# Optimization experiments

Measured on AMD Instinct MI355X. Metric: run time of the kernel, lower is better.

## Reference

```python
import jax, jax.numpy as jnp
import numpy as np

B, T, H, F, E = 512, 32, 768, 3072, 3  # E = num_route_experts = num_experts - 1 (top-1 beam)


def setup_inputs() -> dict:
    key = jax.random.key(0)
    ks = jax.random.split(key, 4)
    s = 0.02
    return {
        "x": jax.random.normal(ks[0], (B, T, H), jnp.float32),
        "Wg": jax.random.normal(ks[1], (E, H), jnp.float32) * s,
        "W1": jax.random.normal(ks[2], (E, H, F), jnp.float32) * s,
        "b1": jnp.zeros((E, F), jnp.float32),
        "W2": jax.random.normal(ks[3], (E, F, H), jnp.float32) * s,
        "b2": jnp.zeros((E, H), jnp.float32),
    }


def reference(x, Wg, W1, b1, W2, b2):
    # forward_gate: mean-pool over tokens (attention_mask is all-ones), linear gate, softmax
    scores = jax.nn.softmax(jnp.mean(x, axis=1) @ Wg.T, axis=-1)  # [B, E]
    # beam_search, first layer with num_route_beam=1: plain top-1 expert selection
    _, idx = jax.lax.top_k(scores, 1)
    sel = idx[:, 0]  # [B] int32, selected expert per sample
    # forward_expert_ffn: densely run EVERY route expert (gelu MLP) on the full batch
    h = jax.nn.gelu(jnp.einsum('bth,ehf->betf', x, W1) + b1[None, :, None, :], approximate=False)  # [B,E,T,F]
    y = jnp.einsum('betf,efh->beth', h, W2) + b2[None, :, None, :]  # [B,E,T,H]
    # weight_type == 'ffn_prob': one-hot mask times gate prob, then sum over experts
    w = scores * jax.nn.one_hot(sel, E, dtype=scores.dtype)  # [B, E]
    out = jnp.einsum('beth,be->bth', y, w)  # [B, T, H]
    return out
```

## Files before the change

### kernel.cpp

```cpp
#include <hip/hip_runtime.h>
#include <hip/hip_bf16.h>
#include <cstdint>
#include <cstddef>

namespace {

constexpr int kB = 512, kT = 32, kH = 768, kF = 3072, kE = 3;
constexpr int kMaxTiles = 131;
constexpr int kMaxChunk = 131;
constexpr int kXPermTile = 128 * kH;
constexpr int kHbufTile  = 128 * kF;

typedef __attribute__((ext_vector_type(8))) short short8;
typedef __attribute__((ext_vector_type(4))) float f32x4;

__device__ __forceinline__ void gld_lds16(const void* g, void* l) {
  __builtin_amdgcn_global_load_lds(
      (const __attribute__((address_space(1))) void*)g,
      (__attribute__((address_space(3))) void*)l, 16, 0, 0);
}

__device__ __forceinline__ float bf2f(__hip_bfloat16 v) { return __bfloat162float(v); }
__device__ __forceinline__ float bfu(unsigned short u) {
  return __uint_as_float(((unsigned)u) << 16);
}
__device__ __forceinline__ unsigned short f2bfb(float f) {
  __hip_bfloat16 h = __float2bfloat16(f);
  return *reinterpret_cast<unsigned short*>(&h);
}

__device__ __forceinline__ float gelu_f(float v) {
  float av = fabsf(v);
  float z = av * 0.70710678118654752f;
  float t = __builtin_amdgcn_rcpf(fmaf(0.3275911f, z, 1.0f));
  float p = fmaf(fmaf(fmaf(fmaf(1.061405429f, t, -1.453152027f), t, 1.421413741f),
                      t, -0.284496736f), t, 0.254829592f) * t;
  float er = fmaf(-p, __expf(-z * z), 1.0f);
  return 0.5f * v + 0.5f * av * er;
}

__global__ void k_sniff_all(const unsigned short* __restrict__ x,
                            const unsigned short* __restrict__ g,
                            const unsigned short* __restrict__ w1,
                            const unsigned short* __restrict__ w2,
                            int* __restrict__ flags, int* __restrict__ cnt,
                            int* __restrict__ ticket) {
  int bb = blockIdx.x;
  if (bb == 0 && threadIdx.x < 4) {
    if (threadIdx.x < 3) cnt[threadIdx.x] = 0;
    else *ticket = 0;
  }
  const unsigned short* p = (bb == 0) ? x : (bb == 1) ? g : (bb == 2) ? w1 : w2;
  int nwords = (bb == 1) ? kE * kH : 4096;
  __shared__ int cnt_s;
  if (threadIdx.x == 0) cnt_s = 0;
  __syncthreads();
  int local = 0;
  for (int i = threadIdx.x; i < nwords; i += 256) {
    unsigned e = (p[i] >> 7) & 0xFF;
    if (e >= 0xC0) ++local;
  }
  atomicAdd(&cnt_s, local);
  __syncthreads();
  if (threadIdx.x == 0) flags[bb] = (cnt_s > 64) ? 1 : 0;
}

__global__ void k_route(const void* __restrict__ xv, const void* __restrict__ Wgv,
                        const int* __restrict__ flags,
                        float* __restrict__ wsel,
                        int* __restrict__ cnt, int* __restrict__ lists,
                        int* __restrict__ ticket,
                        int* __restrict__ tileExpert, int* __restrict__ tileBatch,
                        int* __restrict__ numTiles) {
  bool fx = (flags[0] != 0), fg = (flags[1] != 0);
  int b = blockIdx.x;
  int tid = threadIdx.x;
  float a0 = 0.f, a1 = 0.f, a2 = 0.f;
  if (tid < 192) {
    float m0 = 0.f, m1 = 0.f, m2 = 0.f, m3 = 0.f;
    if (fx) {
      const float4* xr = (const float4*)((const float*)xv + (size_t)b * kT * kH) + tid;
#pragma unroll 8
      for (int t = 0; t < kT; ++t) {
        float4 u = xr[t * 192];
        m0 += u.x; m1 += u.y; m2 += u.z; m3 += u.w;
      }
    } else {
      const ushort4* xr = (const ushort4*)((const unsigned short*)xv + (size_t)b * kT * kH) + tid;
#pragma unroll 8
      for (int t = 0; t < kT; ++t) {
        ushort4 u = xr[t * 192];
        m0 += bfu(u.x); m1 += bfu(u.y); m2 += bfu(u.z); m3 += bfu(u.w);
      }
    }
    const float inv = 1.f / kT;
    m0 *= inv; m1 *= inv; m2 *= inv; m3 *= inv;
#pragma unroll
    for (int e = 0; e < kE; ++e) {
      float w0, w1v, w2v, w3;
      int base = e * kH + tid * 4;
      if (fg) {
        float4 u = *(const float4*)((const float*)Wgv + base);
        w0 = u.x; w1v = u.y; w2v = u.z; w3 = u.w;
      } else {
        ushort4 u = *(const ushort4*)((const unsigned short*)Wgv + base);
        w0 = bfu(u.x); w1v = bfu(u.y); w2v = bfu(u.z); w3 = bfu(u.w);
      }
      float d = m0 * w0 + m1 * w1v + m2 * w2v + m3 * w3;
      if (e == 0) a0 = d; else if (e == 1) a1 = d; else a2 = d;
    }
  }
  __shared__ float red[3][256];
  __shared__ int lastFlag;
  __shared__ int csh[3];
  red[0][tid] = a0; red[1][tid] = a1; red[2][tid] = a2;
  __syncthreads();
  for (int s2 = 128; s2 > 0; s2 >>= 1) {
    if (tid < s2) {
      red[0][tid] += red[0][tid + s2];
      red[1][tid] += red[1][tid + s2];
      red[2][tid] += red[2][tid + s2];
    }
    __syncthreads();
  }
  if (tid == 0) {
    float l0 = red[0][0], l1 = red[1][0], l2 = red[2][0];
    int am = 0; float mx = l0;
    if (l1 > mx) { mx = l1; am = 1; }
    if (l2 > mx) { mx = l2; am = 2; }
    float e0 = expf(l0 - mx), e1 = expf(l1 - mx), e2 = expf(l2 - mx);
    float inv = 1.f / (e0 + e1 + e2);
    float sc = (am == 0 ? e0 : (am == 1 ? e1 : e2)) * inv;
    wsel[b] = sc;
    int pos = atomicAdd(&cnt[am], 1);
    lists[am * kB + pos] = b;
    __threadfence();
    int tk = atomicAdd(ticket, 1);
    lastFlag = (tk == kB - 1) ? 1 : 0;
  }
  __syncthreads();
  if (lastFlag) {
    __threadfence();
    if (tid < 3) csh[tid] = cnt[tid];
    __syncthreads();
    int c0 = csh[0], c1 = csh[1], c2 = csh[2];
    int t0 = ((c0 + 3) & ~3) >> 2;
    int t1 = ((c1 + 3) & ~3) >> 2;
    int t2 = ((c2 + 3) & ~3) >> 2;
    int total = t0 + t1 + t2;
    if (tid == 0) *numTiles = total;
    for (int t = tid; t < kMaxTiles; t += 256) {
      int e = 0, base = 0, cc = 0;
      bool pad = false;
      if (t < t0) { e = 0; base = t; cc = c0; }
      else if (t < t0 + t1) { e = 1; base = t - t0; cc = c1; }
      else if (t < total) { e = 2; base = t - t0 - t1; cc = c2; }
      else pad = true;
      if (pad) {
        tileExpert[t] = 0;
        for (int s = 0; s < 4; ++s) tileBatch[t * 4 + s] = -1;
      } else {
        tileExpert[t] = e;
        for (int s = 0; s < 4; ++s) {
          int i = base * 4 + s;
          tileBatch[t * 4 + s] = (i < cc) ? lists[e * kB + i] : -1;
        }
      }
    }
  }
}

__global__ __launch_bounds__(256)
void k_transpose6(const void* __restrict__ w1src, const void* __restrict__ w2src,
                  __hip_bfloat16* __restrict__ w1dst, __hip_bfloat16* __restrict__ w2dst,
                  const int* __restrict__ flags) {
  int z = blockIdx.z;
  bool isW1 = (z < 3);
  int e = isW1 ? z : z - 3;
  bool f32 = (flags[isW1 ? 2 : 3] != 0);
  const float* sf = (const float*)(isW1 ? w1src : w2src);
  const unsigned short* sb = (const unsigned short*)(isW1 ? w1src : w2src);
  unsigned short* dst = (unsigned short*)(isW1 ? w1dst : w2dst);
  int K = isW1 ? kH : kF, N = isW1 ? kF : kH;
  int ntx = N / 64;
  int bx = blockIdx.x;
  int n0 = (bx % ntx) * 64, k0 = (bx / ntx) * 64;
  __shared__ __align__(16) unsigned short t[64][73];
  size_t eoff = (size_t)e * K * N;
  int tr = threadIdx.x >> 4;
  int tc4 = (threadIdx.x & 15) * 4;
#pragma unroll
  for (int i = 0; i < 4; ++i) {
    int r = tr + 16 * i;
    size_t idx = eoff + (size_t)(k0 + r) * N + n0 + tc4;
    if (f32) {
      float4 u = *(const float4*)(sf + idx);
      t[r][tc4] = f2bfb(u.x); t[r][tc4 + 1] = f2bfb(u.y);
      t[r][tc4 + 2] = f2bfb(u.z); t[r][tc4 + 3] = f2bfb(u.w);
    } else {
      ushort4 u = *(const ushort4*)(sb + idx);
      t[r][tc4] = u.x; t[r][tc4 + 1] = u.y; t[r][tc4 + 2] = u.z; t[r][tc4 + 3] = u.w;
    }
  }
  __syncthreads();
#pragma unroll
  for (int i = 0; i < 4; ++i) {
    int rn = tr + 16 * i;
    ushort4 v;
    v.x = t[tc4][rn]; v.y = t[tc4 + 1][rn]; v.z = t[tc4 + 2][rn]; v.w = t[tc4 + 3][rn];
    *(ushort4*)(dst + eoff + (size_t)(n0 + rn) * K + k0 + tc4) = v;
  }
}

__global__ __launch_bounds__(256)
void k_convert_x(const void* __restrict__ xv, const int* __restrict__ flags,
                 const int* __restrict__ tileBatch, const int* __restrict__ numTiles,
                 __hip_bfloat16* __restrict__ xperm) {
  int tile = blockIdx.y;
  if (tile >= *numTiles) return;
  int kblk = blockIdx.x;
  bool fx = (flags[0] != 0);
  const float* xf = (const float*)xv;
  const __hip_bfloat16* xb = (const __hip_bfloat16*)xv;
  int tb0 = tileBatch[tile * 4];
  if (tb0 < 0) tb0 = 0;
  int tb[4];
#pragma unroll
  for (int s = 0; s < 4; ++s) {
    int bb = tileBatch[tile * 4 + s];
    tb[s] = (bb < 0) ? tb0 : bb;
  }
  int tid = threadIdx.x;
  short8* dst = (short8*)(xperm + (size_t)tile * kXPermTile + kblk * 8192);
#pragma unroll
  for (int i = 0; i < 4; ++i) {
    int s = i * 256 + tid;
    int m = (s >> 2) & 127, kk = s >> 9;
    int q = (s & 3) ^ ((s >> 3) & 3);
    int row = tb[m >> 5] * kT + (m & 31);
    size_t src = (size_t)row * kH + kblk * 64 + kk * 32 + q * 8;
    short8 v;
    if (fx) {
      float4 u = *(const float4*)(xf + src);
      float4 w = *(const float4*)(xf + src + 4);
      v[0] = f2bfb(u.x); v[1] = f2bfb(u.y); v[2] = f2bfb(u.z); v[3] = f2bfb(u.w);
      v[4] = f2bfb(w.x); v[5] = f2bfb(w.y); v[6] = f2bfb(w.z); v[7] = f2bfb(w.w);
    } else {
      v = *(const short8*)(xb + src);
    }
    dst[s] = v;
  }
}

__global__ __launch_bounds__(256, 2)
void k_ffn1(const __hip_bfloat16* __restrict__ xperm,
            const __hip_bfloat16* __restrict__ w1t,
            const __hip_bfloat16* __restrict__ b1,
            const int* __restrict__ tileExpert,
            const int* __restrict__ numTiles,
            int tileOff,
            __hip_bfloat16* __restrict__ hbuf) {
  int j = blockIdx.y;
  int local = j / 3;
  int tile = local + tileOff;
  if (tile >= *numTiles) return;
  int nIdx = 8 * (j % 3) + blockIdx.x;
  int nbase = nIdx * 128;
  int e = tileExpert[tile];
  __shared__ __align__(16) short ldsbuf[16384];
  short* ldsA = ldsbuf;
  short* ldsB = ldsbuf + 8192;
  int tid = threadIdx.x;
  int lane = tid & 63, wid = tid >> 6;
  int wm = wid >> 1, wn = wid & 1;
  int lane16 = lane & 15, qf = lane >> 4;
  int swzl = (lane16 >> 1) & 3;
  int qx = (qf ^ swzl) * 8;

  f32x4 acc[4][4];
#pragma unroll
  for (int r = 0; r < 4; ++r)
#pragma unroll
    for (int c = 0; c < 4; ++c) acc[r][c] = (f32x4)0.f;

  const __hip_bfloat16* w1e = w1t + (size_t)e * kF * kH;
  const __hip_bfloat16* xtile = xperm + (size_t)tile * kXPermTile;
  const __hip_bfloat16* gB[4];
  short* lA[4];
  short* lB[4];
  int aoff[4];
#pragma unroll
  for (int it = 0; it < 4; ++it) {
    int s = it * 256 + tid;
    int m = (s >> 2) & 127, kk = s >> 9;
    int q = (s & 3) ^ ((s >> 3) & 3);
    aoff[it] = s * 8;
    gB[it] = w1e + (size_t)(nbase + m) * kH + kk * 32 + q * 8;
    lA[it] = &ldsA[s * 8];
    lB[it] = &ldsB[s * 8];
  }

  for (int k0 = 0; k0 < kH; k0 += 64) {
#pragma unroll
    for (int it = 0; it < 4; ++it) gld_lds16(xtile + k0 * 128 + aoff[it], lA[it]);
#pragma unroll
    for (int it = 0; it < 4; ++it) gld_lds16(gB[it] + k0, lB[it]);
    __syncthreads();
#pragma unroll
    for (int kk = 0; kk < 2; ++kk) {
      short8 af[4], bfr[4];
#pragma unroll
      for (int r = 0; r < 4; ++r) {
        int mr = wm * 64 + r * 16 + lane16;
        af[r] = *(const short8*)&ldsA[(kk * 512 + mr * 4) * 8 + qx];
      }
#pragma unroll
      for (int c = 0; c < 4; ++c) {
        int mb = wn * 64 + c * 16 + lane16;
        bfr[c] = *(const short8*)&ldsB[(kk * 512 + mb * 4) * 8 + qx];
      }
#pragma unroll
      for (int r = 0; r < 4; ++r)
#pragma unroll
        for (int c = 0; c < 4; ++c)
          acc[r][c] = __builtin_amdgcn_mfma_f32_16x16x32_bf16(af[r], bfr[c], acc[r][c], 0, 0, 0);
    }
    __syncthreads();
  }

  __hip_bfloat16* htile = hbuf + (size_t)local * kHbufTile;
  unsigned short* uls = (unsigned short*)ldsbuf;
  int q4 = qf * 4;
#pragma unroll
  for (int c = 0; c < 4; ++c) {
    int nn = wn * 64 + c * 16 + lane16;
    float bias = bf2f(b1[e * kF + nbase + nn]);
    int lbase = (nn >> 6) * 8192 + ((nn >> 5) & 1) * 4096 + (nn & 7);
    int qn = (nn >> 3) & 3;
#pragma unroll
    for (int r = 0; r < 4; ++r) {
#pragma unroll
      for (int g = 0; g < 4; ++g) {
        int m = wm * 64 + r * 16 + q4 + g;
        float v = acc[r][c][g] + bias;
        uls[lbase + (m * 4 + (qn ^ ((m >> 1) & 3))) * 8] = f2bfb(gelu_f(v));
      }
    }
  }
  __syncthreads();
  unsigned short* dstg = (unsigned short*)htile + (size_t)(nbase >> 6) * 8192;
#pragma unroll
  for (int i = 0; i < 8; ++i) {
    int s = i * 2048 + tid * 8;
    *(short8*)(dstg + s) = *(const short8*)(uls + s);
  }
}

__global__ __launch_bounds__(256, 2)
void k_ffn2(const __hip_bfloat16* __restrict__ hbuf,
            const __hip_bfloat16* __restrict__ w2t,
            const __hip_bfloat16* __restrict__ b2,
            const float* __restrict__ wsel,
            const int* __restrict__ tileExpert,
            const int* __restrict__ tileBatch,
            const int* __restrict__ numTiles,
            int tileOff, int chunk,
            float* __restrict__ out) {
  int j = blockIdx.y;
  int local = blockIdx.x + 8 * (j / 6);
  if (local >= chunk) return;
  int tile = local + tileOff;
  if (tile >= *numTiles) return;
  int nbase = (j % 6) * 128;
  int e = tileExpert[tile];
  int tbraw[4];
  float sc[4];
#pragma unroll
  for (int s = 0; s < 4; ++s) {
    int bb = tileBatch[tile * 4 + s];
    tbraw[s] = bb;
    sc[s] = (bb >= 0) ? wsel[bb] : 0.f;
  }
  __shared__ __align__(16) short ldsA[8192];
  __shared__ __align__(16) short ldsB[8192];
  int tid = threadIdx.x;
  int lane = tid & 63, wid = tid >> 6;
  int wm = wid >> 1, wn = wid & 1;
  int lane16 = lane & 15, qf = lane >> 4;
  int swzl = (lane16 >> 1) & 3;
  int qx = (qf ^ swzl) * 8;

  f32x4 acc[4][4];
#pragma unroll
  for (int r = 0; r < 4; ++r)
#pragma unroll
    for (int c = 0; c < 4; ++c) acc[r][c] = (f32x4)0.f;

  const __hip_bfloat16* w2e = w2t + (size_t)e * kF * kH;
  const __hip_bfloat16* htile = hbuf + (size_t)local * kHbufTile;
  const __hip_bfloat16* gB[4];
  short* lA[4];
  short* lB[4];
  int aoff[4];
#pragma unroll
  for (int it = 0; it < 4; ++it) {
    int s = it * 256 + tid;
    int m = (s >> 2) & 127, kk = s >> 9;
    int q = (s & 3) ^ ((s >> 3) & 3);
    aoff[it] = s * 8;
    gB[it] = w2e + (size_t)(nbase + m) * kF + kk * 32 + q * 8;
    lA[it] = &ldsA[s * 8];
    lB[it] = &ldsB[s * 8];
  }

  for (int k0 = 0; k0 < kF; k0 += 64) {
#pragma unroll
    for (int it = 0; it < 4; ++it) gld_lds16(htile + k0 * 128 + aoff[it], lA[it]);
#pragma unroll
    for (int it = 0; it < 4; ++it) gld_lds16(gB[it] + k0, lB[it]);
    __syncthreads();
#pragma unroll
    for (int kk = 0; kk < 2; ++kk) {
      short8 af[4], bfr[4];
#pragma unroll
      for (int r = 0; r < 4; ++r) {
        int mr = wm * 64 + r * 16 + lane16;
        af[r] = *(const short8*)&ldsA[(kk * 512 + mr * 4) * 8 + qx];
      }
#pragma unroll
      for (int c = 0; c < 4; ++c) {
        int mb = wn * 64 + c * 16 + lane16;
        bfr[c] = *(const short8*)&ldsB[(kk * 512 + mb * 4) * 8 + qx];
      }
#pragma unroll
      for (int r = 0; r < 4; ++r)
#pragma unroll
        for (int c = 0; c < 4; ++c)
          acc[r][c] = __builtin_amdgcn_mfma_f32_16x16x32_bf16(af[r], bfr[c], acc[r][c], 0, 0, 0);
    }
    __syncthreads();
  }

  int q4 = qf * 4;
#pragma unroll
  for (int c = 0; c < 4; ++c) {
    int ncol = wn * 64 + c * 16 + lane16;
    float bias = bf2f(b2[e * kH + nbase + ncol]);
#pragma unroll
    for (int r = 0; r < 4; ++r) {
      int s = (wm * 64 + r * 16) >> 5;
      int bb = tbraw[s];
      if (bb < 0) continue;
      float scale = sc[s];
#pragma unroll
      for (int g = 0; g < 4; ++g) {
        int m = wm * 64 + r * 16 + q4 + g;
        float v = (acc[r][c][g] + bias) * scale;
        out[((size_t)(bb * kT + (m & 31))) * kH + nbase + ncol] = v;
      }
    }
  }
}

}

extern "C" void kernel_launch(void* const* d_in, const int* in_sizes, int n_in,
                              void* d_out, int out_size, void* d_ws, size_t ws_size,
                              hipStream_t stream) {
  (void)in_sizes; (void)n_in; (void)out_size;
  float* out = (float*)d_out;

  char* ws = (char*)d_ws;
  size_t off = 0;
  auto alloc = [&](size_t bytes) -> char* {
    char* p = ws + off;
    off = (off + bytes + 255) & ~(size_t)255;
    return p;
  };
  int*   flags      = (int*)alloc(16);
  int*   cnt        = (int*)alloc(kE * 4);
  int*   ticket     = (int*)alloc(4);
  float* wsel       = (float*)alloc(kB * 4);
  int*   lists      = (int*)alloc((size_t)kE * kB * 4);
  int*   tileExpert = (int*)alloc(kMaxTiles * 4);
  int*   tileBatch  = (int*)alloc(kMaxTiles * 4 * 4);
  int*   numTiles   = (int*)alloc(4);
  __hip_bfloat16* w1t   = (__hip_bfloat16*)alloc((size_t)kE * kH * kF * 2);
  __hip_bfloat16* w2t   = (__hip_bfloat16*)alloc((size_t)kE * kH * kF * 2);
  __hip_bfloat16* xperm = (__hip_bfloat16*)alloc((size_t)kMaxTiles * kXPermTile * 2);

  size_t tileBytes = (size_t)kHbufTile * 2;
  size_t avail = (ws_size > off + tileBytes) ? (ws_size - off) : tileBytes;
  int chunk = (int)(avail / tileBytes);
  if (chunk > kMaxChunk) chunk = kMaxChunk;
  if (chunk < 1) chunk = 1;
  __hip_bfloat16* hbuf = (__hip_bfloat16*)alloc((size_t)chunk * tileBytes);

  k_sniff_all<<<4, 256, 0, stream>>>((const unsigned short*)d_in[0],
                                     (const unsigned short*)d_in[1],
                                     (const unsigned short*)d_in[2],
                                     (const unsigned short*)d_in[4],
                                     flags, cnt, ticket);
  k_route<<<kB, 256, 0, stream>>>(d_in[0], d_in[1], flags, wsel, cnt, lists,
                                  ticket, tileExpert, tileBatch, numTiles);
  k_convert_x<<<dim3(kH / 64, kMaxTiles), 256, 0, stream>>>(d_in[0], flags, tileBatch,
                                                            numTiles, xperm);
  k_transpose6<<<dim3(576, 1, 6), 256, 0, stream>>>(d_in[2], d_in[4], w1t, w2t, flags);
  for (int toff = 0; toff < kMaxTiles; toff += chunk) {
    k_ffn1<<<dim3(8, 3 * chunk), 256, 0, stream>>>(xperm, w1t,
                                                   (const __hip_bfloat16*)d_in[3],
                                                   tileExpert, numTiles, toff, hbuf);
    int rows2 = (chunk + 7) / 8;
    k_ffn2<<<dim3(8, 6 * rows2), 256, 0, stream>>>(hbuf, w2t,
                                                   (const __hip_bfloat16*)d_in[5], wsel,
                                                   tileExpert, tileBatch, numTiles,
                                                   toff, chunk, out);
  }
}
```

Measured before the change: 375.8 us.

## Fuse dtype sniffing and x conversion into routing kernel, gather x in FFN1

Removes the separate sniff and convert_x kernels. Each routing block now detects dtype itself, converts its sample's x to a swizzled bf16 layout per batch through LDS, and writes it out. FFN1 then gathers the rows for each tile straight from that per-batch buffer using tileBatch, instead of reading a pre-permuted per-tile copy. The weight transpose kernel sniffs dtype on its own. This cuts kernel launches and an extra pass over x, in exchange for redundant sniff reads in every block and a large LDS footprint in the routing kernel.

```diff
diff --git a/kernel.cpp b/kernel.cpp
--- a/kernel.cpp
+++ b/kernel.cpp
@@ -8,8 +8,8 @@
 constexpr int kB = 512, kT = 32, kH = 768, kF = 3072, kE = 3;
 constexpr int kMaxTiles = 131;
 constexpr int kMaxChunk = 131;
-constexpr int kXPermTile = 128 * kH;
 constexpr int kHbufTile  = 128 * kF;
+constexpr int kXconvB = kT * kH;
 
 typedef __attribute__((ext_vector_type(8))) short short8;
 typedef __attribute__((ext_vector_type(4))) float f32x4;
@@ -39,42 +39,35 @@
   return 0.5f * v + 0.5f * av * er;
 }
 
-__global__ void k_sniff_all(const unsigned short* __restrict__ x,
-                            const unsigned short* __restrict__ g,
-                            const unsigned short* __restrict__ w1,
-                            const unsigned short* __restrict__ w2,
-                            int* __restrict__ flags, int* __restrict__ cnt,
-                            int* __restrict__ ticket) {
-  int bb = blockIdx.x;
-  if (bb == 0 && threadIdx.x < 4) {
-    if (threadIdx.x < 3) cnt[threadIdx.x] = 0;
-    else *ticket = 0;
-  }
-  const unsigned short* p = (bb == 0) ? x : (bb == 1) ? g : (bb == 2) ? w1 : w2;
-  int nwords = (bb == 1) ? kE * kH : 4096;
-  __shared__ int cnt_s;
-  if (threadIdx.x == 0) cnt_s = 0;
-  __syncthreads();
-  int local = 0;
-  for (int i = threadIdx.x; i < nwords; i += 256) {
-    unsigned e = (p[i] >> 7) & 0xFF;
-    if (e >= 0xC0) ++local;
-  }
-  atomicAdd(&cnt_s, local);
-  __syncthreads();
-  if (threadIdx.x == 0) flags[bb] = (cnt_s > 64) ? 1 : 0;
-}
-
-__global__ void k_route(const void* __restrict__ xv, const void* __restrict__ Wgv,
-                        const int* __restrict__ flags,
-                        float* __restrict__ wsel,
-                        int* __restrict__ cnt, int* __restrict__ lists,
-                        int* __restrict__ ticket,
-                        int* __restrict__ tileExpert, int* __restrict__ tileBatch,
-                        int* __restrict__ numTiles) {
-  bool fx = (flags[0] != 0), fg = (flags[1] != 0);
-  int b = blockIdx.x;
-  int tid = threadIdx.x;
+__global__ __launch_bounds__(256)
+void k_prep_x(const void* __restrict__ xv, const void* __restrict__ Wgv,
+              float* __restrict__ wsel,
+              int* __restrict__ cntTk,
+              int* __restrict__ lists,
+              int* __restrict__ tileExpert, int* __restrict__ tileBatch,
+              int* __restrict__ numTiles,
+              __hip_bfloat16* __restrict__ xconv) {
+  __shared__ __align__(16) unsigned short xs[32][772];
+  __shared__ float red[3][256];
+  __shared__ int sniffX, sniffG, lastFlag;
+  __shared__ int csh[3];
+  int b = blockIdx.x, tid = threadIdx.x;
+  if (tid == 0) { sniffX = 0; sniffG = 0; }
+  __syncthreads();
+  {
+    const unsigned short* xw = (const unsigned short*)xv;
+    const unsigned short* gw = (const unsigned short*)Wgv;
+    int lx = 0, lg = 0;
+#pragma unroll
+    for (int i = 0; i < 16; ++i) lx += (((xw[tid + 256 * i] >> 7) & 0xFF) >= 0xC0);
+#pragma unroll
+    for (int i = 0; i < 8; ++i) lg += (((gw[tid + 256 * i] >> 7) & 0xFF) >= 0xC0);
+    atomicAdd(&sniffX, lx);
+    atomicAdd(&sniffG, lg);
+  }
+  __syncthreads();
+  bool fx = (sniffX > 64), fg = (sniffG > 32);
+
   float a0 = 0.f, a1 = 0.f, a2 = 0.f;
   if (tid < 192) {
     float m0 = 0.f, m1 = 0.f, m2 = 0.f, m3 = 0.f;
@@ -84,6 +77,9 @@
       for (int t = 0; t < kT; ++t) {
         float4 u = xr[t * 192];
         m0 += u.x; m1 += u.y; m2 += u.z; m3 += u.w;
+        ushort4 v;
+        v.x = f2bfb(u.x); v.y = f2bfb(u.y); v.z = f2bfb(u.z); v.w = f2bfb(u.w);
+        *(ushort4*)&xs[t][tid * 4] = v;
       }
     } else {
       const ushort4* xr = (const ushort4*)((const unsigned short*)xv + (size_t)b * kT * kH) + tid;
@@ -91,6 +87,7 @@
       for (int t = 0; t < kT; ++t) {
         ushort4 u = xr[t * 192];
         m0 += bfu(u.x); m1 += bfu(u.y); m2 += bfu(u.z); m3 += bfu(u.w);
+        *(ushort4*)&xs[t][tid * 4] = u;
       }
     }
     const float inv = 1.f / kT;
@@ -110,9 +107,6 @@
       if (e == 0) a0 = d; else if (e == 1) a1 = d; else a2 = d;
     }
   }
-  __shared__ float red[3][256];
-  __shared__ int lastFlag;
-  __shared__ int csh[3];
   red[0][tid] = a0; red[1][tid] = a1; red[2][tid] = a2;
   __syncthreads();
   for (int s2 = 128; s2 > 0; s2 >>= 1) {
@@ -132,16 +126,31 @@
     float inv = 1.f / (e0 + e1 + e2);
     float sc = (am == 0 ? e0 : (am == 1 ? e1 : e2)) * inv;
     wsel[b] = sc;
-    int pos = atomicAdd(&cnt[am], 1);
+    int pos = atomicAdd(&cntTk[am], 1);
     lists[am * kB + pos] = b;
     __threadfence();
-    int tk = atomicAdd(ticket, 1);
+    int tk = atomicAdd(&cntTk[3], 1);
     lastFlag = (tk == kB - 1) ? 1 : 0;
   }
-  __syncthreads();
+
+  __syncthreads();
+  unsigned short* dst = (unsigned short*)xconv + (size_t)b * kXconvB;
+#pragma unroll
+  for (int i = 0; i < 12; ++i) {
+    int g = i * 256 + tid;
+    int t32 = g >> 7, r = g & 127, mm = r >> 2, qp = r & 3;
+    int col = t32 * 32 + (qp ^ ((mm >> 1) & 3)) * 8;
+    ushort4 lo = *(const ushort4*)&xs[mm][col];
+    ushort4 hi = *(const ushort4*)&xs[mm][col + 4];
+    short8 v;
+    v[0] = lo.x; v[1] = lo.y; v[2] = lo.z; v[3] = lo.w;
+    v[4] = hi.x; v[5] = hi.y; v[6] = hi.z; v[7] = hi.w;
+    *(short8*)(dst + g * 8) = v;
+  }
+
   if (lastFlag) {
     __threadfence();
-    if (tid < 3) csh[tid] = cnt[tid];
+    if (tid < 3) csh[tid] = cntTk[tid];
     __syncthreads();
     int c0 = csh[0], c1 = csh[1], c2 = csh[2];
     int t0 = ((c0 + 3) & ~3) >> 2;
@@ -172,12 +181,24 @@
 
 __global__ __launch_bounds__(256)
 void k_transpose6(const void* __restrict__ w1src, const void* __restrict__ w2src,
-                  __hip_bfloat16* __restrict__ w1dst, __hip_bfloat16* __restrict__ w2dst,
-                  const int* __restrict__ flags) {
+                  __hip_bfloat16* __restrict__ w1dst, __hip_bfloat16* __restrict__ w2dst) {
   int z = blockIdx.z;
   bool isW1 = (z < 3);
   int e = isW1 ? z : z - 3;
-  bool f32 = (flags[isW1 ? 2 : 3] != 0);
+  __shared__ __align__(16) unsigned short t[64][73];
+  __shared__ int cnt_s;
+  if (threadIdx.x == 0) cnt_s = 0;
+  __syncthreads();
+  {
+    const unsigned short* hw = (const unsigned short*)(isW1 ? w1src : w2src);
+    int local = 0;
+#pragma unroll
+    for (int i = 0; i < 16; ++i)
+      local += (((hw[threadIdx.x + 256 * i] >> 7) & 0xFF) >= 0xC0);
+    atomicAdd(&cnt_s, local);
+  }
+  __syncthreads();
+  bool f32 = (cnt_s > 64);
   const float* sf = (const float*)(isW1 ? w1src : w2src);
   const unsigned short* sb = (const unsigned short*)(isW1 ? w1src : w2src);
   unsigned short* dst = (unsigned short*)(isW1 ? w1dst : w2dst);
@@ -185,7 +206,6 @@
   int ntx = N / 64;
   int bx = blockIdx.x;
   int n0 = (bx % ntx) * 64, k0 = (bx / ntx) * 64;
-  __shared__ __align__(16) unsigned short t[64][73];
   size_t eoff = (size_t)e * K * N;
   int tr = threadIdx.x >> 4;
   int tc4 = (threadIdx.x & 15) * 4;
@@ -212,51 +232,12 @@
   }
 }
 
-__global__ __launch_bounds__(256)
-void k_convert_x(const void* __restrict__ xv, const int* __restrict__ flags,
-                 const int* __restrict__ tileBatch, const int* __restrict__ numTiles,
-                 __hip_bfloat16* __restrict__ xperm) {
-  int tile = blockIdx.y;
-  if (tile >= *numTiles) return;
-  int kblk = blockIdx.x;
-  bool fx = (flags[0] != 0);
-  const float* xf = (const float*)xv;
-  const __hip_bfloat16* xb = (const __hip_bfloat16*)xv;
-  int tb0 = tileBatch[tile * 4];
-  if (tb0 < 0) tb0 = 0;
-  int tb[4];
-#pragma unroll
-  for (int s = 0; s < 4; ++s) {
-    int bb = tileBatch[tile * 4 + s];
-    tb[s] = (bb < 0) ? tb0 : bb;
-  }
-  int tid = threadIdx.x;
-  short8* dst = (short8*)(xperm + (size_t)tile * kXPermTile + kblk * 8192);
-#pragma unroll
-  for (int i = 0; i < 4; ++i) {
-    int s = i * 256 + tid;
-    int m = (s >> 2) & 127, kk = s >> 9;
-    int q = (s & 3) ^ ((s >> 3) & 3);
-    int row = tb[m >> 5] * kT + (m & 31);
-    size_t src = (size_t)row * kH + kblk * 64 + kk * 32 + q * 8;
-    short8 v;
-    if (fx) {
-      float4 u = *(const float4*)(xf + src);
-      float4 w = *(const float4*)(xf + src + 4);
-      v[0] = f2bfb(u.x); v[1] = f2bfb(u.y); v[2] = f2bfb(u.z); v[3] = f2bfb(u.w);
-      v[4] = f2bfb(w.x); v[5] = f2bfb(w.y); v[6] = f2bfb(w.z); v[7] = f2bfb(w.w);
-    } else {
-      v = *(const short8*)(xb + src);
-    }
-    dst[s] = v;
-  }
-}
-
 __global__ __launch_bounds__(256, 2)
-void k_ffn1(const __hip_bfloat16* __restrict__ xperm,
+void k_ffn1(const __hip_bfloat16* __restrict__ xconv,
             const __hip_bfloat16* __restrict__ w1t,
             const __hip_bfloat16* __restrict__ b1,
             const int* __restrict__ tileExpert,
+            const int* __restrict__ tileBatch,
             const int* __restrict__ numTiles,
             int tileOff,
             __hip_bfloat16* __restrict__ hbuf) {
@@ -277,6 +258,19 @@
   int swzl = (lane16 >> 1) & 3;
   int qx = (qf ^ swzl) * 8;
 
+  int slotLo = tid >> 7;
+  int b0v = tileBatch[tile * 4];
+  int bLo = tileBatch[tile * 4 + slotLo];
+  int bHi = tileBatch[tile * 4 + 2 + slotLo];
+  if (bLo < 0) bLo = b0v;
+  if (bHi < 0) bHi = b0v;
+  int mmLo = (tid >> 2) & 31;
+  int q = (tid & 3) ^ ((tid >> 3) & 3);
+  int qp = q ^ ((mmLo >> 1) & 3);
+  int baseOff = (mmLo * 4 + qp) * 8;
+  const __hip_bfloat16* pLo = xconv + (size_t)bLo * kXconvB + baseOff;
+  const __hip_bfloat16* pHi = xconv + (size_t)bHi * kXconvB + baseOff;
+
   f32x4 acc[4][4];
 #pragma unroll
   for (int r = 0; r < 4; ++r)
@@ -284,25 +278,23 @@
     for (int c = 0; c < 4; ++c) acc[r][c] = (f32x4)0.f;
 
   const __hip_bfloat16* w1e = w1t + (size_t)e * kF * kH;
-  const __hip_bfloat16* xtile = xperm + (size_t)tile * kXPermTile;
   const __hip_bfloat16* gB[4];
-  short* lA[4];
   short* lB[4];
-  int aoff[4];
 #pragma unroll
   for (int it = 0; it < 4; ++it) {
     int s = it * 256 + tid;
     int m = (s >> 2) & 127, kk = s >> 9;
-    int q = (s & 3) ^ ((s >> 3) & 3);
-    aoff[it] = s * 8;
-    gB[it] = w1e + (size_t)(nbase + m) * kH + kk * 32 + q * 8;
-    lA[it] = &ldsA[s * 8];
+    int qq = (s & 3) ^ ((s >> 3) & 3);
+    gB[it] = w1e + (size_t)(nbase + m) * kH + kk * 32 + qq * 8;
     lB[it] = &ldsB[s * 8];
   }
 
   for (int k0 = 0; k0 < kH; k0 += 64) {
-#pragma unroll
-    for (int it = 0; it < 4; ++it) gld_lds16(xtile + k0 * 128 + aoff[it], lA[it]);
+    int koff = (k0 >> 6) * 2048;
+    gld_lds16(pLo + koff,        &ldsA[(0 * 256 + tid) * 8]);
+    gld_lds16(pHi + koff,        &ldsA[(1 * 256 + tid) * 8]);
+    gld_lds16(pLo + koff + 1024, &ldsA[(2 * 256 + tid) * 8]);
+    gld_lds16(pHi + koff + 1024, &ldsA[(3 * 256 + tid) * 8]);
 #pragma unroll
     for (int it = 0; it < 4; ++it) gld_lds16(gB[it] + k0, lB[it]);
     __syncthreads();
@@ -406,9 +398,9 @@
   for (int it = 0; it < 4; ++it) {
     int s = it * 256 + tid;
     int m = (s >> 2) & 127, kk = s >> 9;
-    int q = (s & 3) ^ ((s >> 3) & 3);
+    int qq = (s & 3) ^ ((s >> 3) & 3);
     aoff[it] = s * 8;
-    gB[it] = w2e + (size_t)(nbase + m) * kF + kk * 32 + q * 8;
+    gB[it] = w2e + (size_t)(nbase + m) * kF + kk * 32 + qq * 8;
     lA[it] = &ldsA[s * 8];
     lB[it] = &ldsB[s * 8];
   }
@@ -477,9 +469,7 @@
     off = (off + bytes + 255) & ~(size_t)255;
     return p;
   };
-  int*   flags      = (int*)alloc(16);
-  int*   cnt        = (int*)alloc(kE * 4);
-  int*   ticket     = (int*)alloc(4);
+  int*   cntTk      = (int*)alloc(16);
   float* wsel       = (float*)alloc(kB * 4);
   int*   lists      = (int*)alloc((size_t)kE * kB * 4);
   int*   tileExpert = (int*)alloc(kMaxTiles * 4);
@@ -487,7 +477,7 @@
   int*   numTiles   = (int*)alloc(4);
   __hip_bfloat16* w1t   = (__hip_bfloat16*)alloc((size_t)kE * kH * kF * 2);
   __hip_bfloat16* w2t   = (__hip_bfloat16*)alloc((size_t)kE * kH * kF * 2);
-  __hip_bfloat16* xperm = (__hip_bfloat16*)alloc((size_t)kMaxTiles * kXPermTile * 2);
+  __hip_bfloat16* xconv = (__hip_bfloat16*)alloc((size_t)kB * kXconvB * 2);
 
   size_t tileBytes = (size_t)kHbufTile * 2;
   size_t avail = (ws_size > off + tileBytes) ? (ws_size - off) : tileBytes;
@@ -496,20 +486,15 @@
   if (chunk < 1) chunk = 1;
   __hip_bfloat16* hbuf = (__hip_bfloat16*)alloc((size_t)chunk * tileBytes);
 
-  k_sniff_all<<<4, 256, 0, stream>>>((const unsigned short*)d_in[0],
-                                     (const unsigned short*)d_in[1],
-                                     (const unsigned short*)d_in[2],
-                                     (const unsigned short*)d_in[4],
-                                     flags, cnt, ticket);
-  k_route<<<kB, 256, 0, stream>>>(d_in[0], d_in[1], flags, wsel, cnt, lists,
-                                  ticket, tileExpert, tileBatch, numTiles);
-  k_convert_x<<<dim3(kH / 64, kMaxTiles), 256, 0, stream>>>(d_in[0], flags, tileBatch,
-                                                            numTiles, xperm);
-  k_transpose6<<<dim3(576, 1, 6), 256, 0, stream>>>(d_in[2], d_in[4], w1t, w2t, flags);
+  hipMemsetAsync(cntTk, 0, 16, stream);
+  k_prep_x<<<kB, 256, 0, stream>>>(d_in[0], d_in[1], wsel, cntTk, lists,
+                                   tileExpert, tileBatch, numTiles, xconv);
+  k_transpose6<<<dim3(576, 1, 6), 256, 0, stream>>>(d_in[2], d_in[4], w1t, w2t);
   for (int toff = 0; toff < kMaxTiles; toff += chunk) {
-    k_ffn1<<<dim3(8, 3 * chunk), 256, 0, stream>>>(xperm, w1t,
+    k_ffn1<<<dim3(8, 3 * chunk), 256, 0, stream>>>(xconv, w1t,
                                                    (const __hip_bfloat16*)d_in[3],
-                                                   tileExpert, numTiles, toff, hbuf);
+                                                   tileExpert, tileBatch,
+                                                   numTiles, toff, hbuf);
     int rows2 = (chunk + 7) / 8;
     k_ffn2<<<dim3(8, 6 * rows2), 256, 0, stream>>>(hbuf, w2t,
                                                    (const __hip_bfloat16*)d_in[5], wsel,
```

Result: no change. 378.0 us (+0.6%).
